# Performance work log

Hardware: AMD Instinct MI355X
Metric: run time of the kernel (lower is better)

## Reference

```python
import jax, jax.numpy as jnp
import numpy as np

B, T, DIM, H, D = 4, 2048, 1024, 8, 128
HDIM = H * D


def _rope_tables(t, head_dim):
    # angular_freq: (1/1024)^linspace(0,1,D/4) concatenated with D/4 zeros -> length D/2
    freq = (1.0 / 1024.0) ** jnp.linspace(0.0, 1.0, head_dim // 4)
    freq = jnp.concatenate([freq.astype(jnp.float32), jnp.zeros(head_dim // 4, jnp.float32)])
    theta = jnp.arange(t, dtype=jnp.float32)[:, None] * freq[None, :]  # [T, D/2]
    return jnp.cos(theta), jnp.sin(theta)


def _rms_norm(x):
    # F.rms_norm with no weight, default eps = finfo(dtype).eps
    eps = jnp.finfo(jnp.float32).eps
    return x * jax.lax.rsqrt(jnp.mean(x * x, axis=-1, keepdims=True) + eps)


def _rope(x, cos, sin):
    # x: [B,T,H,D]; rotate-half form matching the torch module
    x1, x2 = jnp.split(x, 2, axis=-1)
    c = cos[None, :, None, :]
    s = sin[None, :, None, :]
    return jnp.concatenate([x1 * c + x2 * s, -x1 * s + x2 * c], axis=-1)


def setup_inputs() -> dict:
    key = jax.random.key(0)
    k0, k1, k2, k3 = jax.random.split(key, 4)
    std = 0.5 * DIM ** -0.5
    bound = (3.0 ** 0.5) * std
    x = jax.random.normal(k0, (B, T, DIM), jnp.float32)
    ve = jax.random.normal(k1, (B, T, HDIM), jnp.float32)
    qkv_w = jax.random.uniform(k2, (3, HDIM, DIM), jnp.float32, -bound, bound)
    lambdas = jnp.array([0.5, 0.5], jnp.float32)
    # c_proj is zero-initialized in the module; use small random weight so output is nontrivial
    c_proj_w = jax.random.uniform(k3, (DIM, HDIM), jnp.float32, -bound, bound)
    return {"x": x, "ve": ve, "qkv_w": qkv_w, "lambdas": lambdas, "c_proj_w": c_proj_w}


def reference(x, ve, qkv_w, lambdas, c_proj_w):
    b, t, dim = x.shape
    hdim = qkv_w.shape[1]
    h, d = hdim // 128, 128
    # fused QKV projection (no bias)
    qkv = (x @ qkv_w.reshape(3 * hdim, dim).T).reshape(b, t, 3 * h, d)
    q, k, v = qkv[:, :, :h], qkv[:, :, h:2 * h], qkv[:, :, 2 * h:]
    # QK RMSNorm then RoPE
    q, k = _rms_norm(q), _rms_norm(k)
    cos, sin = _rope_tables(t, d)
    q, k = _rope(q, cos, sin), _rope(k, cos, sin)
    # lambda-weighted value-embedding mix
    v = lambdas[0] * v + lambdas[1] * ve.reshape(b, t, h, d)
    # naive attention with explicit causal mask (masked_fill -1e9)
    scores = jnp.einsum('bqhd,bkhd->bhqk', q, k) * (d ** -0.5)
    causal = jnp.triu(jnp.ones((t, t), bool), k=1)  # True above diagonal
    scores = jnp.where(causal[None, None], jnp.float32(-1e9), scores)
    probs = jax.nn.softmax(scores, axis=-1)
    y = jnp.einsum('bhqk,bkhd->bqhd', probs, v).reshape(b, t, hdim)
    return y @ c_proj_w.T
```

## Files before the change

kernel.cpp:

```cpp
#include <hip/hip_runtime.h>
#include <hip/hip_bf16.h>

constexpr int B_ = 4;
constexpr int T_ = 2048;
constexpr int DIM_ = 1024;
constexpr int H_ = 8;
constexpr int D_ = 128;
constexpr int HDIM_ = H_ * D_;

typedef __attribute__((ext_vector_type(8))) short bf16x8;
typedef __attribute__((ext_vector_type(8))) unsigned short ushort8;
typedef __attribute__((ext_vector_type(4))) float f32x4;
typedef __attribute__((ext_vector_type(16))) float f32x16;

#define ATTN_SCALE 0.08838834764831845f

__device__ __forceinline__ unsigned short f2bf(float x) {
    unsigned u = __float_as_uint(x);
    unsigned r = (u + 0x7FFFu + ((u >> 16) & 1u)) >> 16;
    return (unsigned short)r;
}
__device__ __forceinline__ float bf2f(unsigned short u) {
    return __uint_as_float(((unsigned)u) << 16);
}

__device__ __forceinline__ void async_ld16(void* ldsdst, const void* gsrc) {
    __builtin_amdgcn_global_load_lds(
        (const __attribute__((address_space(1))) unsigned int*)gsrc,
        (__attribute__((address_space(3))) unsigned int*)ldsdst, 16, 0, 0);
}

__global__ __launch_bounds__(256) void cvtk(const float* __restrict__ in,
                                            unsigned short* __restrict__ out, int n4) {
    int i = blockIdx.x * 256 + threadIdx.x;
    if (i < n4) {
        float4 v = ((const float4*)in)[i];
        ushort4 o;
        o.x = f2bf(v.x); o.y = f2bf(v.y); o.z = f2bf(v.z); o.w = f2bf(v.w);
        ((ushort4*)out)[i] = o;
    }
}

__global__ void rope_tables_k(float* __restrict__ cost, float* __restrict__ sint) {
    int idx = blockIdx.x * blockDim.x + threadIdx.x;
    if (idx >= T_ * 32) return;
    int t = idx >> 5, j = idx & 31;
    float e = (float)j * (1.0f / 31.0f);
    float freq = powf(1.0f / 1024.0f, e);
    float th = (float)t * freq;
    cost[idx] = cosf(th);
    sint[idx] = sinf(th);
}

__global__ __launch_bounds__(256) void gemm_bf16_nt(
    const unsigned short* __restrict__ A, const unsigned short* __restrict__ Bw,
    float* __restrict__ Cf, unsigned short* __restrict__ Cb,
    int M, int N, int K) {
    __shared__ __align__(16) unsigned short As[128 * 64];
    __shared__ __align__(16) unsigned short Bs[128 * 64];
    const int tid = threadIdx.x;
    const int l = tid & 63, w = tid >> 6;
    const int g = l >> 4, q16 = l & 15;

    int nwg = gridDim.x * gridDim.y;
    int lin = blockIdx.y * gridDim.x + blockIdx.x;
    int swz = (lin & 7) * (nwg >> 3) + (lin >> 3);
    int bx = swz % gridDim.x, by = swz / gridDim.x;
    const size_t m0 = (size_t)by * 128, n0 = (size_t)bx * 128;
    const int wm = (w >> 1) * 64, wn = (w & 1) * 64;

    f32x4 acc[4][4];
#pragma unroll
    for (int i = 0; i < 4; ++i)
#pragma unroll
        for (int j = 0; j < 4; ++j) acc[i][j] = (f32x4){0.f, 0.f, 0.f, 0.f};

    const int srow = l >> 3;
    const int schunk = (l & 7) ^ (srow & 7);
    const unsigned short* aBase = A + (m0 + srow) * (size_t)K + schunk * 8;
    const unsigned short* bBase = Bw + (n0 + srow) * (size_t)K + schunk * 8;
    const int roff = q16 & 7;

    for (int k0 = 0; k0 < K; k0 += 64) {
#pragma unroll
        for (int i = 0; i < 4; ++i) {
            size_t rstep = (size_t)(w * 4 + i) * 8 * K;
            async_ld16(&As[(w * 4 + i) * 512], aBase + rstep + k0);
            async_ld16(&Bs[(w * 4 + i) * 512], bBase + rstep + k0);
        }
        __syncthreads();
        __builtin_amdgcn_s_setprio(1);
#pragma unroll
        for (int ks = 0; ks < 2; ++ks) {
            bf16x8 af[4], bf[4];
#pragma unroll
            for (int f = 0; f < 4; ++f) {
                int off = (ks * 32 + g * 8) ^ (roff << 3);
                af[f] = *(const bf16x8*)&As[(wm + f * 16 + q16) * 64 + off];
                bf[f] = *(const bf16x8*)&Bs[(wn + f * 16 + q16) * 64 + off];
            }
#pragma unroll
            for (int fm = 0; fm < 4; ++fm)
#pragma unroll
                for (int fn = 0; fn < 4; ++fn)
                    acc[fm][fn] = __builtin_amdgcn_mfma_f32_16x16x32_bf16(
                        af[fm], bf[fn], acc[fm][fn], 0, 0, 0);
        }
        __builtin_amdgcn_s_setprio(0);
        __syncthreads();
    }

    if (Cb) {
#pragma unroll
        for (int fm = 0; fm < 4; ++fm)
#pragma unroll
            for (int r = 0; r < 4; ++r) {
                size_t base = (m0 + wm + fm * 16 + 4 * g + r) * (size_t)N + n0 + wn + q16;
#pragma unroll
                for (int fn = 0; fn < 4; ++fn)
                    Cb[base + fn * 16] = f2bf(acc[fm][fn][r]);
            }
    } else {
#pragma unroll
        for (int fm = 0; fm < 4; ++fm)
#pragma unroll
            for (int r = 0; r < 4; ++r) {
                size_t base = (m0 + wm + fm * 16 + 4 * g + r) * (size_t)N + n0 + wn + q16;
#pragma unroll
                for (int fn = 0; fn < 4; ++fn)
                    Cf[base + fn * 16] = acc[fm][fn][r];
            }
    }
}

__global__ __launch_bounds__(256) void qkv_prep_k(
    unsigned short* __restrict__ qkv,
    const float* __restrict__ cost, const float* __restrict__ sint) {
    const int gw = (blockIdx.x * 256 + threadIdx.x) >> 6;
    const int lane = threadIdx.x & 63;
    const int h = gw & (H_ - 1);
    const int t = (gw / H_) & (T_ - 1);
    const int b = gw / (H_ * T_);
    const size_t rowbase = ((size_t)(b * T_ + t) * 3) * HDIM_ + (size_t)h * D_;
    const float c = (lane < 32) ? cost[t * 32 + lane] : 1.0f;
    const float s = (lane < 32) ? sint[t * 32 + lane] : 0.0f;
    const float EPS = 1.1920928955078125e-07f;

#pragma unroll
    for (int qk = 0; qk < 2; ++qk) {
        unsigned short* p = qkv + rowbase + (size_t)qk * HDIM_;
        float x1 = bf2f(p[lane]), x2 = bf2f(p[lane + 64]);
        float ss = x1 * x1 + x2 * x2;
#pragma unroll
        for (int m = 32; m >= 1; m >>= 1) ss += __shfl_xor(ss, m, 64);
        float r = 1.0f / sqrtf(ss * (1.0f / 128.0f) + EPS);
        x1 *= r; x2 *= r;
        p[lane]      = f2bf(x1 * c + x2 * s);
        p[lane + 64] = f2bf(x2 * c - x1 * s);
    }
}

__global__ __launch_bounds__(256) void vtrans_k(
    const unsigned short* __restrict__ qkv, const float* __restrict__ ve,
    const float* __restrict__ lambdas, unsigned short* __restrict__ vT) {
    __shared__ unsigned short lds[64][65];
    const int tid = threadIdx.x;
    const int d0 = blockIdx.x * 64, t0 = blockIdx.y * 64;
    const int p = blockIdx.z;
    const int h = p & 7, b = p >> 3;
    const float l0 = lambdas[0], l1 = lambdas[1];

#pragma unroll
    for (int u = 0; u < 2; ++u) {
        int unit = tid + u * 256;
        int i = unit >> 3, jc = (unit & 7) * 8;
        size_t row = (size_t)(b * T_ + t0 + i);
        ushort8 vv = *(const ushort8*)&qkv[(row * 3 + 2) * HDIM_ + h * D_ + d0 + jc];
        const float* pe = &ve[row * HDIM_ + h * D_ + d0 + jc];
        float4 e0 = *(const float4*)pe;
        float4 e1 = *(const float4*)(pe + 4);
        lds[i][jc + 0] = f2bf(l0 * bf2f(vv[0]) + l1 * e0.x);
        lds[i][jc + 1] = f2bf(l0 * bf2f(vv[1]) + l1 * e0.y);
        lds[i][jc + 2] = f2bf(l0 * bf2f(vv[2]) + l1 * e0.z);
        lds[i][jc + 3] = f2bf(l0 * bf2f(vv[3]) + l1 * e0.w);
        lds[i][jc + 4] = f2bf(l0 * bf2f(vv[4]) + l1 * e1.x);
        lds[i][jc + 5] = f2bf(l0 * bf2f(vv[5]) + l1 * e1.y);
        lds[i][jc + 6] = f2bf(l0 * bf2f(vv[6]) + l1 * e1.z);
        lds[i][jc + 7] = f2bf(l0 * bf2f(vv[7]) + l1 * e1.w);
    }
    __syncthreads();
#pragma unroll
    for (int u = 0; u < 2; ++u) {
        int unit = tid + u * 256;
        int r = unit >> 3, tc = (unit & 7) * 8;
        ushort8 o;
#pragma unroll
        for (int m = 0; m < 8; ++m) o[m] = lds[tc + m][r];
        *(ushort8*)&vT[((size_t)(b * H_ + h) * D_ + d0 + r) * T_ + t0 + tc] = o;
    }
}

__global__ __launch_bounds__(256, 2) void attn_mfma(
    const unsigned short* __restrict__ qkv, const unsigned short* __restrict__ vT,
    unsigned short* __restrict__ y) {
    __shared__ __align__(16) unsigned short Ks[2][64 * 128];
    __shared__ __align__(16) unsigned short Vs[2][128 * 64];

    const int tid = threadIdx.x;
    const int l = tid & 63, w = tid >> 6;
    const int l31 = l & 31, hi = l >> 5, l7 = l & 7;
    const int bid = blockIdx.x;
    const int xcd = bid & 7, slot = bid >> 3;
    const int pord = slot >> 4, qo = slot & 15;
    const int p = pord * 8 + xcd;
    const int h = p & 7, b = p >> 3;
    const int qt = (pord < 2) ? (15 - qo) : qo;
    const int q0 = qt * 128;

    const unsigned short* kp[4];
    const unsigned short* vp[4];
#pragma unroll
    for (int i = 0; i < 4; ++i) {
        int r = 16 * w + 4 * i + (l >> 4);
        int kch = (l & 15) ^ (r & 7);
        kp[i] = &qkv[((size_t)(b * T_ + r) * 3 + 1) * HDIM_ + h * D_ + kch * 8];
        int d = 32 * w + 8 * i + (l >> 3);
        int vch = l7 ^ (d & 7);
        vp[i] = &vT[((size_t)(b * H_ + h) * D_ + d) * T_ + vch * 8];
    }
#define STAGE_KV(buf, it_) do {                                        \
        size_t ko_ = (size_t)(it_) * (64 * 3 * HDIM_);                 \
        int vo_ = (it_) * 64;                                          \
        _Pragma("unroll")                                              \
        for (int i_ = 0; i_ < 4; ++i_) {                               \
            async_ld16(&Ks[buf][(w * 4 + i_) * 512], kp[i_] + ko_);    \
            async_ld16(&Vs[buf][(w * 4 + i_) * 512], vp[i_] + vo_);    \
        }                                                              \
    } while (0)

    const int qc = q0 + w * 32 + l31;
    const size_t qbase = ((size_t)(b * T_ + qc) * 3) * HDIM_ + (size_t)h * D_;
    bf16x8 qf[8];
#pragma unroll
    for (int ks = 0; ks < 8; ++ks)
        qf[ks] = *(const bf16x8*)&qkv[qbase + ks * 16 + hi * 8];

    f32x16 accO[4];
#pragma unroll
    for (int i = 0; i < 4; ++i) accO[i] = (f32x16)(0.f);
    float m_s = -1e30f, l_s = 0.f;

    const int nkv = 2 * qt + 2;
    int cur = 0;
    STAGE_KV(0, 0);

    for (int it = 0; it < nkv; ++it) {
        const int kv0 = it * 64;
        __syncthreads();
        if (it + 1 < nkv) STAGE_KV(cur ^ 1, it + 1);

        f32x16 st[2];
        __builtin_amdgcn_s_setprio(1);
#pragma unroll
        for (int mt = 0; mt < 2; ++mt) {
            f32x16 a = (f32x16)(0.f);
            int row = mt * 32 + l31;
#pragma unroll
            for (int ks = 0; ks < 8; ++ks) {
                bf16x8 kf = *(const bf16x8*)&Ks[cur][row * 128 +
                                                     8 * ((2 * ks + hi) ^ l7)];
                a = __builtin_amdgcn_mfma_f32_32x32x16_bf16(kf, qf[ks], a, 0, 0, 0);
            }
            st[mt] = a;
        }
        __builtin_amdgcn_s_setprio(0);

        float sv[2][16];
        float pmax = -1e30f;
        const bool edge = (kv0 + 64 > q0);
#pragma unroll
        for (int mt = 0; mt < 2; ++mt)
#pragma unroll
            for (int r = 0; r < 16; ++r) {
                float x = st[mt][r] * ATTN_SCALE;
                if (edge) {
                    int kvg = kv0 + 32 * mt + (r & 3) + 8 * (r >> 2) + 4 * hi;
                    if (kvg > qc) x = -1e30f;
                }
                sv[mt][r] = x;
                pmax = fmaxf(pmax, x);
            }
        pmax = fmaxf(pmax, __shfl_xor(pmax, 32));

        if (!__all(pmax - m_s <= 8.0f)) {
            float mnew = fmaxf(m_s, pmax);
            float scl = __expf(m_s - mnew);
            m_s = mnew;
            l_s *= scl;
#pragma unroll
            for (int dt = 0; dt < 4; ++dt) accO[dt] *= scl;
        }

        float rsum = 0.f;
#pragma unroll
        for (int mt = 0; mt < 2; ++mt)
#pragma unroll
            for (int r = 0; r < 16; ++r) {
                sv[mt][r] = __expf(sv[mt][r] - m_s);
                rsum += sv[mt][r];
            }
        rsum += __shfl_xor(rsum, 32);
        l_s += rsum;

        bf16x8 pb[4];
#pragma unroll
        for (int mt = 0; mt < 2; ++mt) {
            unsigned w0[4], w1[4], sw0[4], sw1[4];
#pragma unroll
            for (int s = 0; s < 4; ++s) {
                w0[s] = (unsigned)f2bf(sv[mt][4 * s + 0]) |
                        ((unsigned)f2bf(sv[mt][4 * s + 1]) << 16);
                w1[s] = (unsigned)f2bf(sv[mt][4 * s + 2]) |
                        ((unsigned)f2bf(sv[mt][4 * s + 3]) << 16);
            }
#pragma unroll
            for (int s = 0; s < 4; ++s) {
                sw0[s] = __shfl_xor(w0[s], 32);
                sw1[s] = __shfl_xor(w1[s], 32);
            }
#pragma unroll
            for (int ktl = 0; ktl < 2; ++ktl) {
                union { unsigned u[4]; bf16x8 v; } pu;
                pu.u[0] = hi ? sw0[2 * ktl + 1] : w0[2 * ktl];
                pu.u[1] = hi ? sw1[2 * ktl + 1] : w1[2 * ktl];
                pu.u[2] = hi ? w0[2 * ktl + 1] : sw0[2 * ktl];
                pu.u[3] = hi ? w1[2 * ktl + 1] : sw1[2 * ktl];
                pb[mt * 2 + ktl] = pu.v;
            }
        }

        __builtin_amdgcn_s_setprio(1);
#pragma unroll
        for (int dt = 0; dt < 4; ++dt) {
            int drow = dt * 32 + l31;
#pragma unroll
            for (int kt = 0; kt < 4; ++kt) {
                bf16x8 vf = *(const bf16x8*)&Vs[cur][drow * 64 +
                                                     8 * ((2 * kt + hi) ^ l7)];
                accO[dt] = __builtin_amdgcn_mfma_f32_32x32x16_bf16(vf, pb[kt],
                                                                   accO[dt], 0, 0, 0);
            }
        }
        __builtin_amdgcn_s_setprio(0);
        cur ^= 1;
    }
#undef STAGE_KV

    float inv = 1.0f / l_s;
    const size_t yb = (size_t)(b * T_ + qc) * HDIM_ + (size_t)h * D_;
#pragma unroll
    for (int dt = 0; dt < 4; ++dt)
#pragma unroll
        for (int s = 0; s < 4; ++s) {
            ushort4 o;
            o.x = f2bf(accO[dt][4 * s + 0] * inv);
            o.y = f2bf(accO[dt][4 * s + 1] * inv);
            o.z = f2bf(accO[dt][4 * s + 2] * inv);
            o.w = f2bf(accO[dt][4 * s + 3] * inv);
            *(ushort4*)&y[yb + dt * 32 + 8 * s + 4 * hi] = o;
        }
}

extern "C" void kernel_launch(void* const* d_in, const int* in_sizes, int n_in,
                              void* d_out, int out_size, void* d_ws, size_t ws_size,
                              hipStream_t stream) {
    (void)in_sizes; (void)n_in; (void)out_size; (void)ws_size;
    const float* x        = (const float*)d_in[0];
    const float* ve       = (const float*)d_in[1];
    const float* qkv_w    = (const float*)d_in[2];
    const float* lambdas  = (const float*)d_in[3];
    const float* c_proj_w = (const float*)d_in[4];
    float* out = (float*)d_out;

    char* ws = (char*)d_ws;
    unsigned short* qkv = (unsigned short*)ws;
    unsigned short* y   = (unsigned short*)(ws + 50331648);
    unsigned short* xb  = (unsigned short*)(ws + 67108864);
    unsigned short* wb  = (unsigned short*)(ws + 83886080);
    unsigned short* pb  = (unsigned short*)(ws + 90177536);
    float* cost = (float*)(ws + 92274688);
    float* sint = cost + T_ * 32;
    unsigned short* vT  = (unsigned short*)(ws + 100663296);

    hipLaunchKernelGGL(cvtk, dim3(8192), dim3(256), 0, stream, x, xb, 8192 * 1024 / 4);
    hipLaunchKernelGGL(cvtk, dim3(3072), dim3(256), 0, stream, qkv_w, wb, 3072 * 1024 / 4);
    hipLaunchKernelGGL(cvtk, dim3(1024), dim3(256), 0, stream, c_proj_w, pb, 1024 * 1024 / 4);
    hipLaunchKernelGGL(rope_tables_k, dim3(256), dim3(256), 0, stream, cost, sint);

    hipLaunchKernelGGL(gemm_bf16_nt, dim3(24, 64), dim3(256), 0, stream,
                       xb, wb, (float*)nullptr, qkv, B_ * T_, 3 * HDIM_, DIM_);
    hipLaunchKernelGGL(qkv_prep_k, dim3(B_ * T_ * H_ / 4), dim3(256), 0, stream,
                       qkv, cost, sint);
    hipLaunchKernelGGL(vtrans_k, dim3(2, 32, 32), dim3(256), 0, stream,
                       qkv, ve, lambdas, vT);
    hipLaunchKernelGGL(attn_mfma, dim3(512), dim3(256), 0, stream, qkv, vT, y);
    hipLaunchKernelGGL(gemm_bf16_nt, dim3(8, 64), dim3(256), 0, stream,
                       y, pb, out, (unsigned short*)nullptr, B_ * T_, DIM_, HDIM_);
}
```

Baseline: 332.1 us.

## Software-pipeline attention loop: overlap next QK^T with current softmax and PV

```diff
diff --git a/kernel.cpp b/kernel.cpp
--- a/kernel.cpp
+++ b/kernel.cpp
@@ -22,6 +22,11 @@
 }
 __device__ __forceinline__ float bf2f(unsigned short u) {
     return __uint_as_float(((unsigned)u) << 16);
+}
+__device__ __forceinline__ unsigned cvtpk(float lo, float hi_) {
+    unsigned r;
+    asm("v_cvt_pk_bf16_f32 %0, %1, %2" : "=v"(r) : "v"(lo), "v"(hi_));
+    return r;
 }
 
 __device__ __forceinline__ void async_ld16(void* ldsdst, const void* gsrc) {
@@ -155,8 +160,11 @@
         for (int m = 32; m >= 1; m >>= 1) ss += __shfl_xor(ss, m, 64);
         float r = 1.0f / sqrtf(ss * (1.0f / 128.0f) + EPS);
         x1 *= r; x2 *= r;
-        p[lane]      = f2bf(x1 * c + x2 * s);
-        p[lane + 64] = f2bf(x2 * c - x1 * s);
+        float o1 = x1 * c + x2 * s;
+        float o2 = x2 * c - x1 * s;
+        if (qk == 0) { o1 *= ATTN_SCALE; o2 *= ATTN_SCALE; }
+        p[lane]      = f2bf(o1);
+        p[lane + 64] = f2bf(o2);
     }
 }
 
@@ -214,7 +222,7 @@
     const int pord = slot >> 4, qo = slot & 15;
     const int p = pord * 8 + xcd;
     const int h = p & 7, b = p >> 3;
-    const int qt = (pord < 2) ? (15 - qo) : qo;
+    const int qt = 15 - qo;
     const int q0 = qt * 128;
 
     const unsigned short* kp[4];
@@ -228,14 +236,17 @@
         int vch = l7 ^ (d & 7);
         vp[i] = &vT[((size_t)(b * H_ + h) * D_ + d) * T_ + vch * 8];
     }
-#define STAGE_KV(buf, it_) do {                                        \
+#define STAGE_K(buf, it_) do {                                         \
         size_t ko_ = (size_t)(it_) * (64 * 3 * HDIM_);                 \
+        _Pragma("unroll")                                              \
+        for (int i_ = 0; i_ < 4; ++i_)                                 \
+            async_ld16(&Ks[buf][(w * 4 + i_) * 512], kp[i_] + ko_);    \
+    } while (0)
+#define STAGE_V(buf, it_) do {                                         \
         int vo_ = (it_) * 64;                                          \
         _Pragma("unroll")                                              \
-        for (int i_ = 0; i_ < 4; ++i_) {                               \
-            async_ld16(&Ks[buf][(w * 4 + i_) * 512], kp[i_] + ko_);    \
+        for (int i_ = 0; i_ < 4; ++i_)                                 \
             async_ld16(&Vs[buf][(w * 4 + i_) * 512], vp[i_] + vo_);    \
-        }                                                              \
     } while (0)
 
     const int qc = q0 + w * 32 + l31;
@@ -249,112 +260,136 @@
 #pragma unroll
     for (int i = 0; i < 4; ++i) accO[i] = (f32x16)(0.f);
     float m_s = -1e30f, l_s = 0.f;
+    bf16x8 pb[4];
+
+#define QKT_RAW(kbase, S0V, S1V) do {                                        \
+    __builtin_amdgcn_s_setprio(1);                                           \
+    S0V = (f32x16)(0.f); S1V = (f32x16)(0.f);                                \
+    _Pragma("unroll")                                                        \
+    for (int ks_ = 0; ks_ < 8; ++ks_) {                                      \
+        int co_ = 8 * ((2 * ks_ + hi) ^ l7);                                 \
+        bf16x8 k0_ = *(const bf16x8*)&(kbase)[l31 * 128 + co_];              \
+        bf16x8 k1_ = *(const bf16x8*)&(kbase)[(32 + l31) * 128 + co_];       \
+        S0V = __builtin_amdgcn_mfma_f32_32x32x16_bf16(k0_, qf[ks_], S0V, 0, 0, 0); \
+        S1V = __builtin_amdgcn_mfma_f32_32x32x16_bf16(k1_, qf[ks_], S1V, 0, 0, 0); \
+    }                                                                        \
+    __builtin_amdgcn_s_setprio(0);                                           \
+} while (0)
+
+#define PACK_HALF(SV, MT) do {                                               \
+    unsigned w0_[4], w1_[4], sw0_[4], sw1_[4];                               \
+    _Pragma("unroll")                                                        \
+    for (int s_ = 0; s_ < 4; ++s_) {                                         \
+        w0_[s_] = cvtpk(SV[4 * s_ + 0], SV[4 * s_ + 1]);                     \
+        w1_[s_] = cvtpk(SV[4 * s_ + 2], SV[4 * s_ + 3]);                     \
+    }                                                                        \
+    _Pragma("unroll")                                                        \
+    for (int s_ = 0; s_ < 4; ++s_) {                                         \
+        sw0_[s_] = __shfl_xor(w0_[s_], 32);                                  \
+        sw1_[s_] = __shfl_xor(w1_[s_], 32);                                  \
+    }                                                                        \
+    _Pragma("unroll")                                                        \
+    for (int kt_ = 0; kt_ < 2; ++kt_) {                                      \
+        union { unsigned u[4]; bf16x8 v; } pu_;                              \
+        pu_.u[0] = hi ? sw0_[2 * kt_ + 1] : w0_[2 * kt_];                    \
+        pu_.u[1] = hi ? sw1_[2 * kt_ + 1] : w1_[2 * kt_];                    \
+        pu_.u[2] = hi ? w0_[2 * kt_ + 1] : sw0_[2 * kt_];                    \
+        pu_.u[3] = hi ? w1_[2 * kt_ + 1] : sw1_[2 * kt_];                    \
+        pb[(MT) * 2 + kt_] = pu_.v;                                          \
+    }                                                                        \
+} while (0)
+
+#define SM_MASK_PACK(S0V, S1V, kv0_) do {                                    \
+    float sa_[16], sb_[16];                                                  \
+    const bool edge_ = ((kv0_) + 64 > q0);                                   \
+    _Pragma("unroll")                                                        \
+    for (int r_ = 0; r_ < 16; ++r_) {                                        \
+        float x0_ = S0V[r_], x1_ = S1V[r_];                                  \
+        if (edge_) {                                                         \
+            int kg_ = (kv0_) + (r_ & 3) + 8 * (r_ >> 2) + 4 * hi;            \
+            if (kg_ > qc) x0_ = -1e30f;                                      \
+            if (kg_ + 32 > qc) x1_ = -1e30f;                                 \
+        }                                                                    \
+        sa_[r_] = x0_; sb_[r_] = x1_;                                        \
+    }                                                                        \
+    float pm_ = -1e30f;                                                      \
+    _Pragma("unroll")                                                        \
+    for (int r_ = 0; r_ < 16; ++r_)                                          \
+        pm_ = fmaxf(pm_, fmaxf(sa_[r_], sb_[r_]));                           \
+    pm_ = fmaxf(pm_, __shfl_xor(pm_, 32));                                   \
+    if (!__all(pm_ - m_s <= 8.0f)) {                                         \
+        float mn_ = fmaxf(m_s, pm_);                                         \
+        float sc_ = __expf(m_s - mn_);                                       \
+        m_s = mn_; l_s *= sc_;                                               \
+        _Pragma("unroll")                                                    \
+        for (int dt_ = 0; dt_ < 4; ++dt_) accO[dt_] *= sc_;                  \
+    }                                                                        \
+    float rs_ = 0.f;                                                         \
+    _Pragma("unroll")                                                        \
+    for (int r_ = 0; r_ < 16; ++r_) {                                        \
+        sa_[r_] = __expf(sa_[r_] - m_s); rs_ += sa_[r_];                     \
+        sb_[r_] = __expf(sb_[r_] - m_s); rs_ += sb_[r_];                     \
+    }                                                                        \
+    rs_ += __shfl_xor(rs_, 32);                                              \
+    l_s += rs_;                                                              \
+    PACK_HALF(sa_, 0);                                                       \
+    PACK_HALF(sb_, 1);                                                       \
+} while (0)
+
+#define PV_ACC(vbase) do {                                                   \
+    __builtin_amdgcn_s_setprio(1);                                           \
+    _Pragma("unroll")                                                        \
+    for (int dt_ = 0; dt_ < 4; ++dt_) {                                      \
+        int dr_ = dt_ * 32 + l31;                                            \
+        _Pragma("unroll")                                                    \
+        for (int kt_ = 0; kt_ < 4; ++kt_) {                                  \
+            bf16x8 vf_ = *(const bf16x8*)&(vbase)[dr_ * 64 + 8 * ((2 * kt_ + hi) ^ l7)]; \
+            accO[dt_] = __builtin_amdgcn_mfma_f32_32x32x16_bf16(vf_, pb[kt_], accO[dt_], 0, 0, 0); \
+        }                                                                    \
+    }                                                                        \
+    __builtin_amdgcn_s_setprio(0);                                           \
+} while (0)
 
     const int nkv = 2 * qt + 2;
-    int cur = 0;
-    STAGE_KV(0, 0);
-
-    for (int it = 0; it < nkv; ++it) {
-        const int kv0 = it * 64;
+    f32x16 sX0, sX1, sY0, sY1;
+
+    STAGE_K(0, 0);
+    __syncthreads();
+    STAGE_K(1, 1);
+    STAGE_V(0, 0);
+    QKT_RAW(&Ks[0][0], sX0, sX1);
+
+    int t = 1;
+    while (t + 1 < nkv) {
         __syncthreads();
-        if (it + 1 < nkv) STAGE_KV(cur ^ 1, it + 1);
-
-        f32x16 st[2];
-        __builtin_amdgcn_s_setprio(1);
-#pragma unroll
-        for (int mt = 0; mt < 2; ++mt) {
-            f32x16 a = (f32x16)(0.f);
-            int row = mt * 32 + l31;
-#pragma unroll
-            for (int ks = 0; ks < 8; ++ks) {
-                bf16x8 kf = *(const bf16x8*)&Ks[cur][row * 128 +
-                                                     8 * ((2 * ks + hi) ^ l7)];
-                a = __builtin_amdgcn_mfma_f32_32x32x16_bf16(kf, qf[ks], a, 0, 0, 0);
-            }
-            st[mt] = a;
-        }
-        __builtin_amdgcn_s_setprio(0);
-
-        float sv[2][16];
-        float pmax = -1e30f;
-        const bool edge = (kv0 + 64 > q0);
-#pragma unroll
-        for (int mt = 0; mt < 2; ++mt)
-#pragma unroll
-            for (int r = 0; r < 16; ++r) {
-                float x = st[mt][r] * ATTN_SCALE;
-                if (edge) {
-                    int kvg = kv0 + 32 * mt + (r & 3) + 8 * (r >> 2) + 4 * hi;
-                    if (kvg > qc) x = -1e30f;
-                }
-                sv[mt][r] = x;
-                pmax = fmaxf(pmax, x);
-            }
-        pmax = fmaxf(pmax, __shfl_xor(pmax, 32));
-
-        if (!__all(pmax - m_s <= 8.0f)) {
-            float mnew = fmaxf(m_s, pmax);
-            float scl = __expf(m_s - mnew);
-            m_s = mnew;
-            l_s *= scl;
-#pragma unroll
-            for (int dt = 0; dt < 4; ++dt) accO[dt] *= scl;
-        }
-
-        float rsum = 0.f;
-#pragma unroll
-        for (int mt = 0; mt < 2; ++mt)
-#pragma unroll
-            for (int r = 0; r < 16; ++r) {
-                sv[mt][r] = __expf(sv[mt][r] - m_s);
-                rsum += sv[mt][r];
-            }
-        rsum += __shfl_xor(rsum, 32);
-        l_s += rsum;
-
-        bf16x8 pb[4];
-#pragma unroll
-        for (int mt = 0; mt < 2; ++mt) {
-            unsigned w0[4], w1[4], sw0[4], sw1[4];
-#pragma unroll
-            for (int s = 0; s < 4; ++s) {
-                w0[s] = (unsigned)f2bf(sv[mt][4 * s + 0]) |
-                        ((unsigned)f2bf(sv[mt][4 * s + 1]) << 16);
-                w1[s] = (unsigned)f2bf(sv[mt][4 * s + 2]) |
-                        ((unsigned)f2bf(sv[mt][4 * s + 3]) << 16);
-            }
-#pragma unroll
-            for (int s = 0; s < 4; ++s) {
-                sw0[s] = __shfl_xor(w0[s], 32);
-                sw1[s] = __shfl_xor(w1[s], 32);
-            }
-#pragma unroll
-            for (int ktl = 0; ktl < 2; ++ktl) {
-                union { unsigned u[4]; bf16x8 v; } pu;
-                pu.u[0] = hi ? sw0[2 * ktl + 1] : w0[2 * ktl];
-                pu.u[1] = hi ? sw1[2 * ktl + 1] : w1[2 * ktl];
-                pu.u[2] = hi ? w0[2 * ktl + 1] : sw0[2 * ktl];
-                pu.u[3] = hi ? w1[2 * ktl + 1] : sw1[2 * ktl];
-                pb[mt * 2 + ktl] = pu.v;
-            }
-        }
-
-        __builtin_amdgcn_s_setprio(1);
-#pragma unroll
-        for (int dt = 0; dt < 4; ++dt) {
-            int drow = dt * 32 + l31;
-#pragma unroll
-            for (int kt = 0; kt < 4; ++kt) {
-                bf16x8 vf = *(const bf16x8*)&Vs[cur][drow * 64 +
-                                                     8 * ((2 * kt + hi) ^ l7)];
-                accO[dt] = __builtin_amdgcn_mfma_f32_32x32x16_bf16(vf, pb[kt],
-                                                                   accO[dt], 0, 0, 0);
-            }
-        }
-        __builtin_amdgcn_s_setprio(0);
-        cur ^= 1;
-    }
-#undef STAGE_KV
+        STAGE_K(0, t + 1);
+        STAGE_V(1, t);
+        QKT_RAW(&Ks[1][0], sY0, sY1);
+        SM_MASK_PACK(sX0, sX1, (t - 1) * 64);
+        PV_ACC(&Vs[0][0]);
+        __syncthreads();
+        if (t + 2 < nkv) STAGE_K(1, t + 2);
+        STAGE_V(0, t + 1);
+        QKT_RAW(&Ks[0][0], sX0, sX1);
+        SM_MASK_PACK(sY0, sY1, t * 64);
+        PV_ACC(&Vs[1][0]);
+        t += 2;
+    }
+    __syncthreads();
+    STAGE_V(1, t);
+    QKT_RAW(&Ks[1][0], sY0, sY1);
+    SM_MASK_PACK(sX0, sX1, (t - 1) * 64);
+    PV_ACC(&Vs[0][0]);
+    __syncthreads();
+    SM_MASK_PACK(sY0, sY1, t * 64);
+    PV_ACC(&Vs[1][0]);
+
+#undef STAGE_K
+#undef STAGE_V
+#undef QKT_RAW
+#undef PACK_HALF
+#undef SM_MASK_PACK
+#undef PV_ACC
 
     float inv = 1.0f / l_s;
     const size_t yb = (size_t)(b * T_ + qc) * HDIM_ + (size_t)h * D_;
```

Result: no change. 337.2 us (+1.5%).

## Split attention KV tiles across two wave groups and pair causal query tiles per block

Applied to the files above, without the earlier changes.

```diff
diff --git a/kernel.cpp b/kernel.cpp
--- a/kernel.cpp
+++ b/kernel.cpp
@@ -22,6 +22,11 @@
 }
 __device__ __forceinline__ float bf2f(unsigned short u) {
     return __uint_as_float(((unsigned)u) << 16);
+}
+__device__ __forceinline__ unsigned cvtpk(float lo, float hi_) {
+    unsigned r;
+    asm("v_cvt_pk_bf16_f32 %0, %1, %2" : "=v"(r) : "v"(lo), "v"(hi_));
+    return r;
 }
 
 __device__ __forceinline__ void async_ld16(void* ldsdst, const void* gsrc) {
@@ -155,8 +160,11 @@
         for (int m = 32; m >= 1; m >>= 1) ss += __shfl_xor(ss, m, 64);
         float r = 1.0f / sqrtf(ss * (1.0f / 128.0f) + EPS);
         x1 *= r; x2 *= r;
-        p[lane]      = f2bf(x1 * c + x2 * s);
-        p[lane + 64] = f2bf(x2 * c - x1 * s);
+        float o1 = x1 * c + x2 * s;
+        float o2 = x2 * c - x1 * s;
+        if (qk == 0) { o1 *= ATTN_SCALE; o2 *= ATTN_SCALE; }
+        p[lane]      = f2bf(o1);
+        p[lane + 64] = f2bf(o2);
     }
 }
 
@@ -200,175 +208,186 @@
     }
 }
 
-__global__ __launch_bounds__(256, 2) void attn_mfma(
+__global__ __launch_bounds__(512, 2) void attn_mfma(
     const unsigned short* __restrict__ qkv, const unsigned short* __restrict__ vT,
     unsigned short* __restrict__ y) {
-    __shared__ __align__(16) unsigned short Ks[2][64 * 128];
-    __shared__ __align__(16) unsigned short Vs[2][128 * 64];
+    __shared__ __align__(16) unsigned short smem[2][2][64 * 128];
+    __shared__ float mlm[4][32], mll[4][32];
 
     const int tid = threadIdx.x;
     const int l = tid & 63, w = tid >> 6;
     const int l31 = l & 31, hi = l >> 5, l7 = l & 7;
+    const int qg = w & 3, half = w >> 2;
     const int bid = blockIdx.x;
     const int xcd = bid & 7, slot = bid >> 3;
-    const int pord = slot >> 4, qo = slot & 15;
+    const int pord = slot >> 3, qp = slot & 7;
     const int p = pord * 8 + xcd;
     const int h = p & 7, b = p >> 3;
-    const int qt = (pord < 2) ? (15 - qo) : qo;
-    const int q0 = qt * 128;
-
-    const unsigned short* kp[4];
-    const unsigned short* vp[4];
-#pragma unroll
-    for (int i = 0; i < 4; ++i) {
-        int r = 16 * w + 4 * i + (l >> 4);
+
+    const unsigned short* kp[2];
+    const unsigned short* vp[2];
+#pragma unroll
+    for (int i = 0; i < 2; ++i) {
+        int r = 8 * w + 4 * i + (l >> 4);
         int kch = (l & 15) ^ (r & 7);
         kp[i] = &qkv[((size_t)(b * T_ + r) * 3 + 1) * HDIM_ + h * D_ + kch * 8];
-        int d = 32 * w + 8 * i + (l >> 3);
+        int d = 16 * w + 8 * i + (l >> 3);
         int vch = l7 ^ (d & 7);
         vp[i] = &vT[((size_t)(b * H_ + h) * D_ + d) * T_ + vch * 8];
     }
-#define STAGE_KV(buf, it_) do {                                        \
-        size_t ko_ = (size_t)(it_) * (64 * 3 * HDIM_);                 \
-        int vo_ = (it_) * 64;                                          \
-        _Pragma("unroll")                                              \
-        for (int i_ = 0; i_ < 4; ++i_) {                               \
-            async_ld16(&Ks[buf][(w * 4 + i_) * 512], kp[i_] + ko_);    \
-            async_ld16(&Vs[buf][(w * 4 + i_) * 512], vp[i_] + vo_);    \
-        }                                                              \
+#define STAGE(bufi, it_) do {                                              \
+        size_t ko_ = (size_t)(it_) * (64 * 3 * HDIM_);                     \
+        int vo_ = (it_) * 64;                                              \
+        _Pragma("unroll")                                                  \
+        for (int i_ = 0; i_ < 2; ++i_) {                                   \
+            async_ld16(&smem[bufi][0][(w * 2 + i_) * 512], kp[i_] + ko_);  \
+            async_ld16(&smem[bufi][1][(w * 2 + i_) * 512], vp[i_] + vo_);  \
+        }                                                                  \
     } while (0)
 
-    const int qc = q0 + w * 32 + l31;
-    const size_t qbase = ((size_t)(b * T_ + qc) * 3) * HDIM_ + (size_t)h * D_;
-    bf16x8 qf[8];
-#pragma unroll
-    for (int ks = 0; ks < 8; ++ks)
-        qf[ks] = *(const bf16x8*)&qkv[qbase + ks * 16 + hi * 8];
-
-    f32x16 accO[4];
-#pragma unroll
-    for (int i = 0; i < 4; ++i) accO[i] = (f32x16)(0.f);
-    float m_s = -1e30f, l_s = 0.f;
-
-    const int nkv = 2 * qt + 2;
-    int cur = 0;
-    STAGE_KV(0, 0);
-
-    for (int it = 0; it < nkv; ++it) {
-        const int kv0 = it * 64;
+    for (int pass = 0; pass < 2; ++pass) {
+        const int qt = pass ? (15 - qp) : qp;
+        const int q0 = qt * 128;
+        const int qc = q0 + qg * 32 + l31;
+        const size_t qbase = ((size_t)(b * T_ + qc) * 3) * HDIM_ + (size_t)h * D_;
+        bf16x8 qf[8];
+#pragma unroll
+        for (int ks = 0; ks < 8; ++ks)
+            qf[ks] = *(const bf16x8*)&qkv[qbase + ks * 16 + hi * 8];
+
+        f32x16 accO[4];
+#pragma unroll
+        for (int i = 0; i < 4; ++i) accO[i] = (f32x16)(0.f);
+        float m_s = -1e30f, l_s = 0.f;
+        bf16x8 pb[2];
+
+        const int nkv = 2 * qt + 2;
+        int cur = 0;
+        STAGE(0, 0);
+
+        for (int t = 0; t < nkv; ++t) {
+            __syncthreads();
+            if (t + 1 < nkv) STAGE(cur ^ 1, t + 1);
+
+            const unsigned short* Kb = &smem[cur][0][0];
+            const int row = half * 32 + l31;
+            f32x16 S = (f32x16)(0.f);
+            __builtin_amdgcn_s_setprio(1);
+#pragma unroll
+            for (int ks = 0; ks < 8; ++ks) {
+                bf16x8 kf = *(const bf16x8*)&Kb[row * 128 + 8 * ((2 * ks + hi) ^ l7)];
+                S = __builtin_amdgcn_mfma_f32_32x32x16_bf16(kf, qf[ks], S, 0, 0, 0);
+            }
+            __builtin_amdgcn_s_setprio(0);
+
+            float sv[16];
+            float pmax = -1e30f;
+            const int kvbase = t * 64 + half * 32;
+            const bool edge = (kvbase + 32 > q0 + qg * 32);
+#pragma unroll
+            for (int r = 0; r < 16; ++r) {
+                float x = S[r];
+                if (edge) {
+                    int kg = kvbase + (r & 3) + 8 * (r >> 2) + 4 * hi;
+                    if (kg > qc) x = -1e30f;
+                }
+                sv[r] = x;
+                pmax = fmaxf(pmax, x);
+            }
+            pmax = fmaxf(pmax, __shfl_xor(pmax, 32));
+            if (!__all(pmax - m_s <= 8.0f)) {
+                float mn = fmaxf(m_s, pmax);
+                float sc = __expf(m_s - mn);
+                m_s = mn; l_s *= sc;
+#pragma unroll
+                for (int dt = 0; dt < 4; ++dt) accO[dt] *= sc;
+            }
+            float rs = 0.f;
+#pragma unroll
+            for (int r = 0; r < 16; ++r) {
+                sv[r] = __expf(sv[r] - m_s);
+                rs += sv[r];
+            }
+            rs += __shfl_xor(rs, 32);
+            l_s += rs;
+
+            {
+                unsigned w0[4], w1[4], sw0[4], sw1[4];
+#pragma unroll
+                for (int s = 0; s < 4; ++s) {
+                    w0[s] = cvtpk(sv[4 * s + 0], sv[4 * s + 1]);
+                    w1[s] = cvtpk(sv[4 * s + 2], sv[4 * s + 3]);
+                }
+#pragma unroll
+                for (int s = 0; s < 4; ++s) {
+                    sw0[s] = __shfl_xor(w0[s], 32);
+                    sw1[s] = __shfl_xor(w1[s], 32);
+                }
+#pragma unroll
+                for (int kt = 0; kt < 2; ++kt) {
+                    union { unsigned u[4]; bf16x8 v; } pu;
+                    pu.u[0] = hi ? sw0[2 * kt + 1] : w0[2 * kt];
+                    pu.u[1] = hi ? sw1[2 * kt + 1] : w1[2 * kt];
+                    pu.u[2] = hi ? w0[2 * kt + 1] : sw0[2 * kt];
+                    pu.u[3] = hi ? w1[2 * kt + 1] : sw1[2 * kt];
+                    pb[kt] = pu.v;
+                }
+            }
+
+            const unsigned short* Vb = &smem[cur][1][0];
+            __builtin_amdgcn_s_setprio(1);
+#pragma unroll
+            for (int dt = 0; dt < 4; ++dt) {
+                int dr = dt * 32 + l31;
+#pragma unroll
+                for (int kt = 0; kt < 2; ++kt) {
+                    int ktg = half * 2 + kt;
+                    bf16x8 vf = *(const bf16x8*)&Vb[dr * 64 + 8 * ((2 * ktg + hi) ^ l7)];
+                    accO[dt] = __builtin_amdgcn_mfma_f32_32x32x16_bf16(vf, pb[kt],
+                                                                       accO[dt], 0, 0, 0);
+                }
+            }
+            __builtin_amdgcn_s_setprio(0);
+            cur ^= 1;
+        }
+
         __syncthreads();
-        if (it + 1 < nkv) STAGE_KV(cur ^ 1, it + 1);
-
-        f32x16 st[2];
-        __builtin_amdgcn_s_setprio(1);
-#pragma unroll
-        for (int mt = 0; mt < 2; ++mt) {
-            f32x16 a = (f32x16)(0.f);
-            int row = mt * 32 + l31;
-#pragma unroll
-            for (int ks = 0; ks < 8; ++ks) {
-                bf16x8 kf = *(const bf16x8*)&Ks[cur][row * 128 +
-                                                     8 * ((2 * ks + hi) ^ l7)];
-                a = __builtin_amdgcn_mfma_f32_32x32x16_bf16(kf, qf[ks], a, 0, 0, 0);
-            }
-            st[mt] = a;
+        float* Cb = (float*)&smem[0][0][0];
+        if (half == 0) {
+            mlm[qg][l31] = m_s;
+            mll[qg][l31] = l_s;
+#pragma unroll
+            for (int dt = 0; dt < 4; ++dt)
+#pragma unroll
+                for (int r = 0; r < 16; ++r) {
+                    int d = dt * 32 + (r & 3) + 8 * (r >> 2) + 4 * hi;
+                    Cb[(qg * 32 + l31) * 128 + d] = accO[dt][r];
+                }
         }
-        __builtin_amdgcn_s_setprio(0);
-
-        float sv[2][16];
-        float pmax = -1e30f;
-        const bool edge = (kv0 + 64 > q0);
-#pragma unroll
-        for (int mt = 0; mt < 2; ++mt)
-#pragma unroll
-            for (int r = 0; r < 16; ++r) {
-                float x = st[mt][r] * ATTN_SCALE;
-                if (edge) {
-                    int kvg = kv0 + 32 * mt + (r & 3) + 8 * (r >> 2) + 4 * hi;
-                    if (kvg > qc) x = -1e30f;
-                }
-                sv[mt][r] = x;
-                pmax = fmaxf(pmax, x);
-            }
-        pmax = fmaxf(pmax, __shfl_xor(pmax, 32));
-
-        if (!__all(pmax - m_s <= 8.0f)) {
-            float mnew = fmaxf(m_s, pmax);
-            float scl = __expf(m_s - mnew);
-            m_s = mnew;
-            l_s *= scl;
-#pragma unroll
-            for (int dt = 0; dt < 4; ++dt) accO[dt] *= scl;
+        __syncthreads();
+        if (half == 1) {
+            float mA = mlm[qg][l31], lA = mll[qg][l31];
+            float mM = fmaxf(mA, m_s);
+            float sA = __expf(mA - mM), sB = __expf(m_s - mM);
+            float linv = 1.0f / (sA * lA + sB * l_s);
+            const size_t yb = (size_t)(b * T_ + qc) * HDIM_ + (size_t)h * D_;
+            const float* Crow = &Cb[(qg * 32 + l31) * 128];
+#pragma unroll
+            for (int dt = 0; dt < 4; ++dt)
+#pragma unroll
+                for (int s = 0; s < 4; ++s) {
+                    int d0 = dt * 32 + 8 * s + 4 * hi;
+                    ushort4 o;
+                    o.x = f2bf((sA * Crow[d0 + 0] + sB * accO[dt][4 * s + 0]) * linv);
+                    o.y = f2bf((sA * Crow[d0 + 1] + sB * accO[dt][4 * s + 1]) * linv);
+                    o.z = f2bf((sA * Crow[d0 + 2] + sB * accO[dt][4 * s + 2]) * linv);
+                    o.w = f2bf((sA * Crow[d0 + 3] + sB * accO[dt][4 * s + 3]) * linv);
+                    *(ushort4*)&y[yb + d0] = o;
+                }
         }
-
-        float rsum = 0.f;
-#pragma unroll
-        for (int mt = 0; mt < 2; ++mt)
-#pragma unroll
-            for (int r = 0; r < 16; ++r) {
-                sv[mt][r] = __expf(sv[mt][r] - m_s);
-                rsum += sv[mt][r];
-            }
-        rsum += __shfl_xor(rsum, 32);
-        l_s += rsum;
-
-        bf16x8 pb[4];
-#pragma unroll
-        for (int mt = 0; mt < 2; ++mt) {
-            unsigned w0[4], w1[4], sw0[4], sw1[4];
-#pragma unroll
-            for (int s = 0; s < 4; ++s) {
-                w0[s] = (unsigned)f2bf(sv[mt][4 * s + 0]) |
-                        ((unsigned)f2bf(sv[mt][4 * s + 1]) << 16);
-                w1[s] = (unsigned)f2bf(sv[mt][4 * s + 2]) |
-                        ((unsigned)f2bf(sv[mt][4 * s + 3]) << 16);
-            }
-#pragma unroll
-            for (int s = 0; s < 4; ++s) {
-                sw0[s] = __shfl_xor(w0[s], 32);
-                sw1[s] = __shfl_xor(w1[s], 32);
-            }
-#pragma unroll
-            for (int ktl = 0; ktl < 2; ++ktl) {
-                union { unsigned u[4]; bf16x8 v; } pu;
-                pu.u[0] = hi ? sw0[2 * ktl + 1] : w0[2 * ktl];
-                pu.u[1] = hi ? sw1[2 * ktl + 1] : w1[2 * ktl];
-                pu.u[2] = hi ? w0[2 * ktl + 1] : sw0[2 * ktl];
-                pu.u[3] = hi ? w1[2 * ktl + 1] : sw1[2 * ktl];
-                pb[mt * 2 + ktl] = pu.v;
-            }
-        }
-
-        __builtin_amdgcn_s_setprio(1);
-#pragma unroll
-        for (int dt = 0; dt < 4; ++dt) {
-            int drow = dt * 32 + l31;
-#pragma unroll
-            for (int kt = 0; kt < 4; ++kt) {
-                bf16x8 vf = *(const bf16x8*)&Vs[cur][drow * 64 +
-                                                     8 * ((2 * kt + hi) ^ l7)];
-                accO[dt] = __builtin_amdgcn_mfma_f32_32x32x16_bf16(vf, pb[kt],
-                                                                   accO[dt], 0, 0, 0);
-            }
-        }
-        __builtin_amdgcn_s_setprio(0);
-        cur ^= 1;
-    }
-#undef STAGE_KV
-
-    float inv = 1.0f / l_s;
-    const size_t yb = (size_t)(b * T_ + qc) * HDIM_ + (size_t)h * D_;
-#pragma unroll
-    for (int dt = 0; dt < 4; ++dt)
-#pragma unroll
-        for (int s = 0; s < 4; ++s) {
-            ushort4 o;
-            o.x = f2bf(accO[dt][4 * s + 0] * inv);
-            o.y = f2bf(accO[dt][4 * s + 1] * inv);
-            o.z = f2bf(accO[dt][4 * s + 2] * inv);
-            o.w = f2bf(accO[dt][4 * s + 3] * inv);
-            *(ushort4*)&y[yb + dt * 32 + 8 * s + 4 * hi] = o;
-        }
+        __syncthreads();
+    }
+#undef STAGE
 }
 
 extern "C" void kernel_launch(void* const* d_in, const int* in_sizes, int n_in,
@@ -403,7 +422,7 @@
                        qkv, cost, sint);
     hipLaunchKernelGGL(vtrans_k, dim3(2, 32, 32), dim3(256), 0, stream,
                        qkv, ve, lambdas, vT);
-    hipLaunchKernelGGL(attn_mfma, dim3(512), dim3(256), 0, stream, qkv, vT, y);
+    hipLaunchKernelGGL(attn_mfma, dim3(256), dim3(512), 0, stream, qkv, vT, y);
     hipLaunchKernelGGL(gemm_bf16_nt, dim3(8, 64), dim3(256), 0, stream,
                        y, pb, out, (unsigned short*)nullptr, B_ * T_, DIM_, HDIM_);
 }
```

Result: faster. 312.3 us (-6.0%).
